# Performance work log

Measured on AMD Instinct MI355X. Metric: run time of the kernel, lower is better.

The kernel has to match this reference:

```python
import jax, jax.numpy as jnp
import numpy as np

C = 768
N = 2048
BS = 8
MASK_VAL = 1e10


def _sincos(n, c):
    # torch sinusoidal_position_embedding: interleaved sin/cos, then
    # cos_pos = emb[..., 1::2].repeat_interleave(2), sin_pos = emb[..., ::2].repeat_interleave(2)
    pos = jnp.arange(n, dtype=jnp.float32)[:, None]            # [N,1]
    inv = jnp.power(10000.0, -2.0 * jnp.arange(c // 2, dtype=jnp.float32) / c)  # [C/2]
    ang = pos * inv                                            # [N, C/2]
    sin = jnp.repeat(jnp.sin(ang), 2, axis=-1)                 # [N, C]
    cos = jnp.repeat(jnp.cos(ang), 2, axis=-1)                 # [N, C]
    return sin[None], cos[None]                                # [1, N, C]


def _rope(x, sin, cos):
    # x2 = interleave(-x_odd, x_even)
    x2 = jnp.stack([-x[..., 1::2], x[..., ::2]], axis=-1).reshape(x.shape)
    return x * cos + x2 * sin


def _global_pointer(x, Wq, bq, Wk, bk, sin, cos, mask):
    xq = jnp.einsum('bnc,dc->bnd', x, Wq) + bq
    xk = jnp.einsum('bnc,dc->bnd', x, Wk) + bk
    xq = _rope(xq, sin, cos)
    xk = _rope(xk, sin, cos)
    logits = jnp.einsum('bnd,bmd->bnm', xq, xk)
    logits = logits - mask * MASK_VAL
    return logits / jnp.sqrt(jnp.float32(C))


def setup_inputs() -> dict:
    key = jax.random.key(0)
    ks = jax.random.split(key, 9)
    s = 0.02
    return {
        'feature': jax.random.normal(ks[0], (BS, N, C), jnp.float32),
        'Wq': jax.random.normal(ks[1], (C, C), jnp.float32) * s,
        'bq': jax.random.normal(ks[2], (C,), jnp.float32) * s,
        'Wk': jax.random.normal(ks[3], (C, C), jnp.float32) * s,
        'bk': jax.random.normal(ks[4], (C,), jnp.float32) * s,
        'Wq_cls': jax.random.normal(ks[5], (C, C), jnp.float32) * s,
        'bq_cls': jax.random.normal(ks[6], (C,), jnp.float32) * s,
        'Wk_cls': jax.random.normal(ks[7], (C, C), jnp.float32) * s,
        'bk_cls': jax.random.normal(ks[8], (C,), jnp.float32) * s,
    }


def reference(feature, Wq, bq, Wk, bk, Wq_cls, bq_cls, Wk_cls, bk_cls):
    n = feature.shape[1]
    sin, cos = _sincos(n, C)
    mask = jnp.tril(jnp.ones((n, n), jnp.float32), k=-1)  # strictly lower triangular
    gp = _global_pointer(feature, Wq, bq, Wk, bk, sin, cos, mask)
    gp_cls = _global_pointer(feature, Wq_cls, bq_cls, Wk_cls, bk_cls, sin, cos, mask)
    # stacked: [2, bs, N, N] = (global_pointer, global_pointer_cls)
    return jnp.stack([gp, gp_cls], axis=0)
```

## Files before the change

kernel.cpp:

```cpp
#include <hip/hip_runtime.h>
#include <hip/hip_bf16.h>
#include <stdint.h>

typedef unsigned short u16;
typedef __attribute__((ext_vector_type(8))) __bf16 bf16x8;
typedef __attribute__((ext_vector_type(4))) float f32x4;

#define C_DIM 768
#define HALF_C 384
#define N_SEQ 2048
#define BATCH 8
#define M_TOT (BATCH * N_SEQ)
#define BK 32
#define NT (C_DIM / BK)

__device__ __forceinline__ u16 f2bf(float f) {
    union { float f; unsigned u; } c; c.f = f;
    unsigned r = (c.u + 0x7FFFu + ((c.u >> 16) & 1u)) >> 16;
    return (u16)r;
}

#define PREP_XBLK 12288
#define PREP_WBLK 576
#define PREP_SBLK 3072
__global__ __launch_bounds__(256) void prep_kernel(
    const float* __restrict__ feat,
    const float* __restrict__ Wq, const float* __restrict__ Wk,
    const float* __restrict__ Wqc, const float* __restrict__ Wkc,
    u16* __restrict__ xbf,
    u16* __restrict__ w0, u16* __restrict__ w1,
    u16* __restrict__ w2, u16* __restrict__ w3,
    uint32_t* __restrict__ cs_tab) {
    const int b = blockIdx.x, tid = threadIdx.x;
    if (b < PREP_XBLK + 4 * PREP_WBLK) {
        const float* src; u16* dst; int base;
        if (b < PREP_XBLK)                    { src = feat; dst = xbf; base = 0; }
        else if (b < PREP_XBLK + PREP_WBLK)   { src = Wq;  dst = w0; base = PREP_XBLK; }
        else if (b < PREP_XBLK + 2*PREP_WBLK) { src = Wk;  dst = w1; base = PREP_XBLK + PREP_WBLK; }
        else if (b < PREP_XBLK + 3*PREP_WBLK) { src = Wqc; dst = w2; base = PREP_XBLK + 2*PREP_WBLK; }
        else                                  { src = Wkc; dst = w3; base = PREP_XBLK + 3*PREP_WBLK; }
        const int i = (b - base) * 256 + tid;
        float4 v = ((const float4*)src)[i];
        ushort4 o;
        o.x = f2bf(v.x); o.y = f2bf(v.y); o.z = f2bf(v.z); o.w = f2bf(v.w);
        ((ushort4*)dst)[i] = o;
    } else {
        const int idx = (b - PREP_XBLK - 4 * PREP_WBLK) * 256 + tid;
        const int ip  = idx >> 11;
        const int pos = idx & (N_SEQ - 1);
        float inv = powf(10000.0f, (-2.0f / (float)C_DIM) * (float)ip);
        float ang = (float)pos * inv;
        uint32_t c = f2bf(cosf(ang)), s = f2bf(sinf(ang));
        cs_tab[idx] = (s << 16) | c;
    }
}

template<int N> __device__ __forceinline__ void vmwait();
template<> __device__ __forceinline__ void vmwait<8>() { asm volatile("s_waitcnt vmcnt(8)" ::: "memory"); }
template<> __device__ __forceinline__ void vmwait<4>() { asm volatile("s_waitcnt vmcnt(4)" ::: "memory"); }
template<> __device__ __forceinline__ void vmwait<0>() { asm volatile("s_waitcnt vmcnt(0)" ::: "memory"); }

__device__ __forceinline__ void async_load16(const void* src, void* dst_lds) {
    const __attribute__((address_space(1))) void* g =
        (const __attribute__((address_space(1))) void*)(uintptr_t)src;
    __attribute__((address_space(3))) void* l =
        (__attribute__((address_space(3))) void*)(unsigned)(uintptr_t)dst_lds;
    __builtin_amdgcn_global_load_lds(g, l, 16, 0, 0);
}

__device__ __forceinline__ void stage32(const u16* __restrict__ gbase, int ld,
                                        u16* ldsbase, int wave, int lane) {
    const int s  = (lane & 3) ^ ((lane >> 4) & 3);
    const int rr = lane >> 2;
    #pragma unroll
    for (int j = 0; j < 2; ++j) {
        const int chunk = wave * 2 + j;
        const u16* src = gbase + (size_t)(chunk * 16 + rr) * ld + s * 8;
        u16* dst = ldsbase + chunk * 512;
        async_load16(src, dst);
    }
}

__device__ __forceinline__ void gemm256_mainloop(
    const u16* __restrict__ A, const u16* __restrict__ B, int ld,
    u16* LdsA, u16* LdsB, f32x4 (&acc)[8][4], int wave, int lane) {

    #pragma unroll
    for (int t = 0; t < 3; ++t) {
        stage32(A + t * BK, ld, LdsA + t * 8192, wave, lane);
        stage32(B + t * BK, ld, LdsB + t * 8192, wave, lane);
    }
    __builtin_amdgcn_sched_barrier(0);
    vmwait<8>();
    __builtin_amdgcn_s_barrier();
    __builtin_amdgcn_sched_barrier(0);

    const int r = lane & 15, sl = lane >> 4;
    const int lane_off = r * 32 + ((sl ^ ((r >> 2) & 3)) * 8);
    const int wm = wave >> 2, wn = wave & 3;
    const int a_base = lane_off + wm * 512;
    const int b_base = lane_off + wn * 512;

    #pragma unroll
    for (int t = 0; t < NT; ++t) {
        const u16* At = LdsA + (t & 3) * 8192;
        const u16* Bt = LdsB + (t & 3) * 8192;
        bf16x8 a[4], b[4], a2[4];

        if (t + 3 < NT) stage32(A + (t + 3) * BK, ld, LdsA + ((t + 3) & 3) * 8192, wave, lane);
        #pragma unroll
        for (int mf = 0; mf < 4; ++mf) a[mf] = *(const bf16x8*)(At + a_base + mf * 1024);
        #pragma unroll
        for (int nf = 0; nf < 4; ++nf) b[nf] = *(const bf16x8*)(Bt + b_base + nf * 2048);
        __builtin_amdgcn_sched_barrier(0);
        __builtin_amdgcn_s_barrier();
        __builtin_amdgcn_sched_barrier(0);
        __builtin_amdgcn_s_setprio(1);
        #pragma unroll
        for (int mf = 0; mf < 4; ++mf)
            #pragma unroll
            for (int nf = 0; nf < 4; ++nf)
                acc[mf][nf] = __builtin_amdgcn_mfma_f32_16x16x32_bf16(a[mf], b[nf], acc[mf][nf], 0, 0, 0);
        __builtin_amdgcn_s_setprio(0);
        __builtin_amdgcn_sched_barrier(0);
        __builtin_amdgcn_s_barrier();
        __builtin_amdgcn_sched_barrier(0);

        if (t + 3 < NT) stage32(B + (t + 3) * BK, ld, LdsB + ((t + 3) & 3) * 8192, wave, lane);
        #pragma unroll
        for (int mf = 0; mf < 4; ++mf) a2[mf] = *(const bf16x8*)(At + a_base + (mf + 4) * 1024);
        __builtin_amdgcn_sched_barrier(0);
        __builtin_amdgcn_s_barrier();
        __builtin_amdgcn_sched_barrier(0);
        __builtin_amdgcn_s_setprio(1);
        #pragma unroll
        for (int mf = 0; mf < 4; ++mf)
            #pragma unroll
            for (int nf = 0; nf < 4; ++nf)
                acc[mf + 4][nf] = __builtin_amdgcn_mfma_f32_16x16x32_bf16(a2[mf], b[nf], acc[mf + 4][nf], 0, 0, 0);
        __builtin_amdgcn_s_setprio(0);
        __builtin_amdgcn_sched_barrier(0);
        if (t <= NT - 4)      vmwait<8>();
        else if (t == NT - 3) vmwait<4>();
        else if (t == NT - 2) vmwait<0>();
        __builtin_amdgcn_s_barrier();
        __builtin_amdgcn_sched_barrier(0);
    }
}

__global__ __launch_bounds__(512, 2) void proj_kernel(
    const u16* __restrict__ xbf,
    const u16* __restrict__ W0, const u16* __restrict__ W1,
    const u16* __restrict__ W2, const u16* __restrict__ W3,
    const float* __restrict__ b0, const float* __restrict__ b1,
    const float* __restrict__ b2, const float* __restrict__ b3,
    u16* __restrict__ o0, u16* __restrict__ o1, u16* __restrict__ o2, u16* __restrict__ o3,
    const uint32_t* __restrict__ cs_tab) {
    __shared__ __align__(16) u16 LdsA[4 * 8192];
    __shared__ __align__(16) u16 LdsB[4 * 8192];
    const int tid = threadIdx.x, lane = tid & 63, wave = tid >> 6;
    const int bid = blockIdx.x;
    const int xcd = bid & 7, widx = bid >> 3;
    const int bx  = xcd * 8 + (widx & 7);
    const int t2  = widx >> 3;
    const int z   = t2 / 3;
    const int by  = t2 - z * 3;
    const int m0 = bx * 256, n0 = by * 256;

    const u16*   W    = z == 0 ? W0 : z == 1 ? W1 : z == 2 ? W2 : W3;
    const float* bias = z == 0 ? b0 : z == 1 ? b1 : z == 2 ? b2 : b3;
    u16*         outp = z == 0 ? o0 : z == 1 ? o1 : z == 2 ? o2 : o3;

    f32x4 acc[8][4];
    #pragma unroll
    for (int x = 0; x < 8; ++x)
        #pragma unroll
        for (int y = 0; y < 4; ++y) acc[x][y] = f32x4{0.f, 0.f, 0.f, 0.f};

    gemm256_mainloop(xbf + (size_t)m0 * C_DIM, W + (size_t)n0 * C_DIM, C_DIM,
                     LdsA, LdsB, acc, wave, lane);

    const int wm = wave >> 2, wn = wave & 3;
    const int g = lane >> 4, r = lane & 15;
    #pragma unroll
    for (int nf = 0; nf < 4; ++nf) {
        const int col = n0 + wn * 64 + nf * 16 + r;
        const float bv = bias[col];
        const float sgn = (col & 1) ? 1.0f : -1.0f;
        const uint32_t* csrow = cs_tab + (size_t)(col >> 1) * N_SEQ;
        #pragma unroll
        for (int mf = 0; mf < 8; ++mf) {
            const int rowb = m0 + mf * 32 + wm * 16 + g * 4;
            const uint4 cs4 = *(const uint4*)(csrow + (rowb & (N_SEQ - 1)));
            #pragma unroll
            for (int i = 0; i < 4; ++i) {
                const int row = rowb + i;
                float v = acc[mf][nf][i] + bv;
                float p = __shfl_xor(v, 1);
                const uint32_t cs = ((const uint32_t*)&cs4)[i];
                const float c = __uint_as_float(cs << 16);
                const float s = __uint_as_float(cs & 0xFFFF0000u);
                outp[(size_t)row * C_DIM + col] = f2bf(v * c + sgn * p * s);
            }
        }
    }
}

__global__ __launch_bounds__(512, 2) void logits_kernel(
    const u16* __restrict__ Q0, const u16* __restrict__ K0,
    const u16* __restrict__ Q1, const u16* __restrict__ K1,
    float* __restrict__ out) {
    __shared__ __align__(16) u16 LdsA[4 * 8192];
    __shared__ __align__(16) u16 LdsB[4 * 8192];
    const int tid = threadIdx.x, lane = tid & 63, wave = tid >> 6;
    const int bid = blockIdx.x;
    const int swz = (bid & 7) * 128 + (bid >> 3);
    const int z   = swz >> 6;
    const int rem = swz & 63;
    const int by  = rem >> 3;
    const int bx  = rem & 7;
    const int nrow0 = by * 256, mcol0 = bx * 256;

    const float RS = 0.036084391824351613f;
    const float MV = 1.0e10f * RS;
    float* outz = out + (size_t)z * N_SEQ * N_SEQ;

    if (bx < by) {
        const float4 cv = {-MV, -MV, -MV, -MV};
        #pragma unroll
        for (int i = 0; i < 32; ++i) {
            const int row = nrow0 + wave * 32 + i;
            *(float4*)(outz + (size_t)row * N_SEQ + mcol0 + lane * 4) = cv;
        }
        return;
    }

    const int h = z >> 3, b = z & 7;
    const u16* Qb = (h ? Q1 : Q0) + (size_t)b * N_SEQ * C_DIM;
    const u16* Kb = (h ? K1 : K0) + (size_t)b * N_SEQ * C_DIM;

    f32x4 acc[8][4];
    #pragma unroll
    for (int x = 0; x < 8; ++x)
        #pragma unroll
        for (int y = 0; y < 4; ++y) acc[x][y] = f32x4{0.f, 0.f, 0.f, 0.f};

    gemm256_mainloop(Qb + (size_t)nrow0 * C_DIM, Kb + (size_t)mcol0 * C_DIM, C_DIM,
                     LdsA, LdsB, acc, wave, lane);

    const int wm = wave >> 2, wn = wave & 3;
    const int g = lane >> 4, r = lane & 15;
    #pragma unroll
    for (int mf = 0; mf < 8; ++mf) {
        #pragma unroll
        for (int i = 0; i < 4; ++i) {
            const int row = nrow0 + mf * 32 + wm * 16 + g * 4 + i;
            float* orow = outz + (size_t)row * N_SEQ;
            #pragma unroll
            for (int nf = 0; nf < 4; ++nf) {
                const int col = mcol0 + wn * 64 + nf * 16 + r;
                orow[col] = acc[mf][nf][i] * RS - (col < row ? MV : 0.0f);
            }
        }
    }
}

extern "C" void kernel_launch(void* const* d_in, const int* in_sizes, int n_in,
                              void* d_out, int out_size, void* d_ws, size_t ws_size,
                              hipStream_t stream) {
    (void)in_sizes; (void)n_in; (void)out_size; (void)ws_size;
    const float* feat = (const float*)d_in[0];
    const float* Wq   = (const float*)d_in[1];
    const float* bq   = (const float*)d_in[2];
    const float* Wk   = (const float*)d_in[3];
    const float* bk   = (const float*)d_in[4];
    const float* Wqc  = (const float*)d_in[5];
    const float* bqc  = (const float*)d_in[6];
    const float* Wkc  = (const float*)d_in[7];
    const float* bkc  = (const float*)d_in[8];
    float* out = (float*)d_out;

    u16* ws = (u16*)d_ws;
    const size_t XE = (size_t)M_TOT * C_DIM;
    const size_t WE = (size_t)C_DIM * C_DIM;
    u16* xbf = ws;
    u16* Wb0 = ws + XE;
    u16* Wb1 = Wb0 + WE;
    u16* Wb2 = Wb1 + WE;
    u16* Wb3 = Wb2 + WE;
    u16* qkbase = Wb3 + WE;
    u16* Qa = qkbase;
    u16* Ka = qkbase + XE;
    u16* Qc = qkbase + 2 * XE;
    u16* Kc = qkbase + 3 * XE;
    uint32_t* cs_tab = (uint32_t*)(qkbase + 4 * XE);

    prep_kernel<<<dim3(PREP_XBLK + 4 * PREP_WBLK + PREP_SBLK), dim3(256), 0, stream>>>(
        feat, Wq, Wk, Wqc, Wkc, xbf, Wb0, Wb1, Wb2, Wb3, cs_tab);

    proj_kernel<<<dim3(768), dim3(512), 0, stream>>>(
        xbf, Wb0, Wb1, Wb2, Wb3, bq, bk, bqc, bkc, Qa, Ka, Qc, Kc, cs_tab);

    logits_kernel<<<dim3(1024), dim3(512), 0, stream>>>(
        Qa, Ka, Qc, Kc, out);
}
```

Measured before the change: 237.4 us.

## Widen projection tiles to 256x384 with triple-buffered LDS and staged coalesced stores

The projection GEMM tile grows from 256x256 to 256x384, so each block holds 8x6 accumulators and the grid shrinks from 768 to 512 blocks, which is exactly two per CU. The LDS pipeline moves from four stages of separate A/B buffers to three combined slots, with prefetch depth two and adjusted vmcnt waits. The RoPE epilogue now writes bf16 results into swizzled LDS in two halves and then stores them to global memory as coalesced 16-byte vectors, replacing scattered 2-byte stores. The intent is better operand reuse, a single full wave of blocks, and cheaper output writes. The cost is higher register pressure and a shallower prefetch pipeline.

After: 240.5 us. No clear change (+1.3%).

```diff
diff --git a/kernel.cpp b/kernel.cpp
--- a/kernel.cpp
+++ b/kernel.cpp
@@ -57,6 +57,7 @@
 
 template<int N> __device__ __forceinline__ void vmwait();
 template<> __device__ __forceinline__ void vmwait<8>() { asm volatile("s_waitcnt vmcnt(8)" ::: "memory"); }
+template<> __device__ __forceinline__ void vmwait<5>() { asm volatile("s_waitcnt vmcnt(5)" ::: "memory"); }
 template<> __device__ __forceinline__ void vmwait<4>() { asm volatile("s_waitcnt vmcnt(4)" ::: "memory"); }
 template<> __device__ __forceinline__ void vmwait<0>() { asm volatile("s_waitcnt vmcnt(0)" ::: "memory"); }
 
@@ -68,16 +69,16 @@
     __builtin_amdgcn_global_load_lds(g, l, 16, 0, 0);
 }
 
-__device__ __forceinline__ void stage32(const u16* __restrict__ gbase, int ld,
-                                        u16* ldsbase, int wave, int lane) {
+template<int NCHUNK>
+__device__ __forceinline__ void stageN(const u16* __restrict__ gbase, int ld,
+                                       u16* ldsbase, int wave, int lane) {
     const int s  = (lane & 3) ^ ((lane >> 4) & 3);
     const int rr = lane >> 2;
     #pragma unroll
-    for (int j = 0; j < 2; ++j) {
-        const int chunk = wave * 2 + j;
+    for (int j = 0; j < NCHUNK; ++j) {
+        const int chunk = wave * NCHUNK + j;
         const u16* src = gbase + (size_t)(chunk * 16 + rr) * ld + s * 8;
-        u16* dst = ldsbase + chunk * 512;
-        async_load16(src, dst);
+        async_load16(src, ldsbase + chunk * 512);
     }
 }
 
@@ -87,8 +88,8 @@
 
     #pragma unroll
     for (int t = 0; t < 3; ++t) {
-        stage32(A + t * BK, ld, LdsA + t * 8192, wave, lane);
-        stage32(B + t * BK, ld, LdsB + t * 8192, wave, lane);
+        stageN<2>(A + t * BK, ld, LdsA + t * 8192, wave, lane);
+        stageN<2>(B + t * BK, ld, LdsB + t * 8192, wave, lane);
     }
     __builtin_amdgcn_sched_barrier(0);
     vmwait<8>();
@@ -107,7 +108,7 @@
         const u16* Bt = LdsB + (t & 3) * 8192;
         bf16x8 a[4], b[4], a2[4];
 
-        if (t + 3 < NT) stage32(A + (t + 3) * BK, ld, LdsA + ((t + 3) & 3) * 8192, wave, lane);
+        if (t + 3 < NT) stageN<2>(A + (t + 3) * BK, ld, LdsA + ((t + 3) & 3) * 8192, wave, lane);
         #pragma unroll
         for (int mf = 0; mf < 4; ++mf) a[mf] = *(const bf16x8*)(At + a_base + mf * 1024);
         #pragma unroll
@@ -126,7 +127,7 @@
         __builtin_amdgcn_s_barrier();
         __builtin_amdgcn_sched_barrier(0);
 
-        if (t + 3 < NT) stage32(B + (t + 3) * BK, ld, LdsB + ((t + 3) & 3) * 8192, wave, lane);
+        if (t + 3 < NT) stageN<2>(B + (t + 3) * BK, ld, LdsB + ((t + 3) & 3) * 8192, wave, lane);
         #pragma unroll
         for (int mf = 0; mf < 4; ++mf) a2[mf] = *(const bf16x8*)(At + a_base + (mf + 4) * 1024);
         __builtin_amdgcn_sched_barrier(0);
@@ -148,6 +149,7 @@
     }
 }
 
+#define PSLOT 20480
 __global__ __launch_bounds__(512, 2) void proj_kernel(
     const u16* __restrict__ xbf,
     const u16* __restrict__ W0, const u16* __restrict__ W1,
@@ -156,53 +158,130 @@
     const float* __restrict__ b2, const float* __restrict__ b3,
     u16* __restrict__ o0, u16* __restrict__ o1, u16* __restrict__ o2, u16* __restrict__ o3,
     const uint32_t* __restrict__ cs_tab) {
-    __shared__ __align__(16) u16 LdsA[4 * 8192];
-    __shared__ __align__(16) u16 LdsB[4 * 8192];
+    __shared__ __align__(16) u16 Lds[3 * PSLOT];
     const int tid = threadIdx.x, lane = tid & 63, wave = tid >> 6;
     const int bid = blockIdx.x;
     const int xcd = bid & 7, widx = bid >> 3;
     const int bx  = xcd * 8 + (widx & 7);
     const int t2  = widx >> 3;
-    const int z   = t2 / 3;
-    const int by  = t2 - z * 3;
-    const int m0 = bx * 256, n0 = by * 256;
+    const int z   = t2 >> 1;
+    const int by  = t2 & 1;
+    const int m0 = bx * 256, n0 = by * 384;
 
     const u16*   W    = z == 0 ? W0 : z == 1 ? W1 : z == 2 ? W2 : W3;
     const float* bias = z == 0 ? b0 : z == 1 ? b1 : z == 2 ? b2 : b3;
     u16*         outp = z == 0 ? o0 : z == 1 ? o1 : z == 2 ? o2 : o3;
-
-    f32x4 acc[8][4];
+    const u16* A = xbf + (size_t)m0 * C_DIM;
+    const u16* B = W + (size_t)n0 * C_DIM;
+
+    f32x4 acc[8][6];
     #pragma unroll
     for (int x = 0; x < 8; ++x)
         #pragma unroll
-        for (int y = 0; y < 4; ++y) acc[x][y] = f32x4{0.f, 0.f, 0.f, 0.f};
-
-    gemm256_mainloop(xbf + (size_t)m0 * C_DIM, W + (size_t)n0 * C_DIM, C_DIM,
-                     LdsA, LdsB, acc, wave, lane);
-
+        for (int y = 0; y < 6; ++y) acc[x][y] = f32x4{0.f, 0.f, 0.f, 0.f};
+
+    #pragma unroll
+    for (int t = 0; t < 2; ++t) {
+        stageN<2>(A + t * BK, C_DIM, Lds + t * PSLOT, wave, lane);
+        stageN<3>(B + t * BK, C_DIM, Lds + t * PSLOT + 8192, wave, lane);
+    }
+    __builtin_amdgcn_sched_barrier(0);
+    vmwait<5>();
+    __builtin_amdgcn_s_barrier();
+    __builtin_amdgcn_sched_barrier(0);
+
+    const int r = lane & 15, sl = lane >> 4;
+    const int lane_off = r * 32 + ((sl ^ ((r >> 2) & 3)) * 8);
     const int wm = wave >> 2, wn = wave & 3;
-    const int g = lane >> 4, r = lane & 15;
-    #pragma unroll
-    for (int nf = 0; nf < 4; ++nf) {
-        const int col = n0 + wn * 64 + nf * 16 + r;
-        const float bv = bias[col];
-        const float sgn = (col & 1) ? 1.0f : -1.0f;
-        const uint32_t* csrow = cs_tab + (size_t)(col >> 1) * N_SEQ;
-        #pragma unroll
-        for (int mf = 0; mf < 8; ++mf) {
-            const int rowb = m0 + mf * 32 + wm * 16 + g * 4;
-            const uint4 cs4 = *(const uint4*)(csrow + (rowb & (N_SEQ - 1)));
-            #pragma unroll
-            for (int i = 0; i < 4; ++i) {
-                const int row = rowb + i;
-                float v = acc[mf][nf][i] + bv;
-                float p = __shfl_xor(v, 1);
-                const uint32_t cs = ((const uint32_t*)&cs4)[i];
-                const float c = __uint_as_float(cs << 16);
-                const float s = __uint_as_float(cs & 0xFFFF0000u);
-                outp[(size_t)row * C_DIM + col] = f2bf(v * c + sgn * p * s);
+    const int a_base = lane_off + wm * 512;
+    const int b_base = 8192 + lane_off + wn * 3072;
+
+    #pragma unroll
+    for (int t = 0; t < NT; ++t) {
+        const u16* S = Lds + (t % 3) * PSLOT;
+        u16* D = Lds + ((t + 2) % 3) * PSLOT;
+        bf16x8 a[4], b[6], a2[4];
+
+        if (t + 2 < NT) stageN<2>(A + (t + 2) * BK, C_DIM, D, wave, lane);
+        #pragma unroll
+        for (int mf = 0; mf < 4; ++mf) a[mf] = *(const bf16x8*)(S + a_base + mf * 1024);
+        #pragma unroll
+        for (int nf = 0; nf < 6; ++nf) b[nf] = *(const bf16x8*)(S + b_base + nf * 512);
+        __builtin_amdgcn_sched_barrier(0);
+        __builtin_amdgcn_s_barrier();
+        __builtin_amdgcn_sched_barrier(0);
+        __builtin_amdgcn_s_setprio(1);
+        #pragma unroll
+        for (int mf = 0; mf < 4; ++mf)
+            #pragma unroll
+            for (int nf = 0; nf < 6; ++nf)
+                acc[mf][nf] = __builtin_amdgcn_mfma_f32_16x16x32_bf16(a[mf], b[nf], acc[mf][nf], 0, 0, 0);
+        __builtin_amdgcn_s_setprio(0);
+        __builtin_amdgcn_sched_barrier(0);
+        __builtin_amdgcn_s_barrier();
+        __builtin_amdgcn_sched_barrier(0);
+
+        if (t + 2 < NT) stageN<3>(B + (t + 2) * BK, C_DIM, D + 8192, wave, lane);
+        #pragma unroll
+        for (int mf = 0; mf < 4; ++mf) a2[mf] = *(const bf16x8*)(S + a_base + (mf + 4) * 1024);
+        __builtin_amdgcn_sched_barrier(0);
+        __builtin_amdgcn_s_barrier();
+        __builtin_amdgcn_sched_barrier(0);
+        __builtin_amdgcn_s_setprio(1);
+        #pragma unroll
+        for (int mf = 0; mf < 4; ++mf)
+            #pragma unroll
+            for (int nf = 0; nf < 6; ++nf)
+                acc[mf + 4][nf] = __builtin_amdgcn_mfma_f32_16x16x32_bf16(a2[mf], b[nf], acc[mf + 4][nf], 0, 0, 0);
+        __builtin_amdgcn_s_setprio(0);
+        __builtin_amdgcn_sched_barrier(0);
+        if (t < NT - 2)       vmwait<5>();
+        else if (t == NT - 2) vmwait<0>();
+        __builtin_amdgcn_s_barrier();
+        __builtin_amdgcn_sched_barrier(0);
+    }
+
+    const int g = lane >> 4;
+    #pragma unroll
+    for (int h = 0; h < 2; ++h) {
+        #pragma unroll
+        for (int nf3 = 0; nf3 < 3; ++nf3) {
+            const int nf = 3 * h + nf3;
+            const int colL = wn * 96 + nf * 16 + r;
+            const int col  = n0 + colL;
+            const float bv = bias[col];
+            const float sgn = (col & 1) ? 1.0f : -1.0f;
+            const uint32_t* csrow = cs_tab + (size_t)(col >> 1) * N_SEQ;
+            const int cidx = wn * 48 + nf3 * 16 + r;
+            #pragma unroll
+            for (int mf = 0; mf < 8; ++mf) {
+                const int rowb = m0 + mf * 32 + wm * 16 + g * 4;
+                const uint4 cs4 = *(const uint4*)(csrow + (rowb & (N_SEQ - 1)));
+                #pragma unroll
+                for (int i = 0; i < 4; ++i) {
+                    float v = acc[mf][nf][i] + bv;
+                    float p = __shfl_xor(v, 1);
+                    const uint32_t cs = ((const uint32_t*)&cs4)[i];
+                    const float c = __uint_as_float(cs << 16);
+                    const float s = __uint_as_float(cs & 0xFFFF0000u);
+                    const int rowL = mf * 32 + wm * 16 + g * 4 + i;
+                    const int ba = rowL * 384 + ((cidx * 2) ^ (((rowL >> 2) & 3) << 5));
+                    *(u16*)((char*)Lds + ba) = f2bf(v * c + sgn * p * s);
+                }
             }
         }
+        __syncthreads();
+        #pragma unroll
+        for (int k = 0; k < 12; ++k) {
+            const int f = (k * 512 + tid) * 16;
+            const int row = f / 384;
+            const int inrow = f - row * 384;
+            const uint4 vv = *(const uint4*)((const char*)Lds + row * 384 + (inrow ^ (((row >> 2) & 3) << 5)));
+            const int c8 = inrow >> 1;
+            const int gcol = (c8 / 48) * 96 + h * 48 + (c8 % 48);
+            *(uint4*)(outp + (size_t)(m0 + row) * C_DIM + n0 + gcol) = vv;
+        }
+        __syncthreads();
     }
 }
 
@@ -298,7 +377,7 @@
     prep_kernel<<<dim3(PREP_XBLK + 4 * PREP_WBLK + PREP_SBLK), dim3(256), 0, stream>>>(
         feat, Wq, Wk, Wqc, Wkc, xbf, Wb0, Wb1, Wb2, Wb3, cs_tab);
 
-    proj_kernel<<<dim3(768), dim3(512), 0, stream>>>(
+    proj_kernel<<<dim3(512), dim3(512), 0, stream>>>(
         xbf, Wb0, Wb1, Wb2, Wb3, bq, bk, bqc, bkc, Qa, Ka, Qc, Kc, cs_tab);
 
     logits_kernel<<<dim3(1024), dim3(512), 0, stream>>>(
```
